# Optimization experiments

Hardware: AMD Instinct MI355X
Metric: run time of the kernel (lower is better)

The kernel has to match this reference:

```python
import jax, jax.numpy as jnp
import numpy as np
from functools import partial

N_NODES = 50000
N_EDGES = 600000
N_FEAT = 128
HID = [128, 64, 32, 16]
N_GRAPHS = 64
N_CLASSES = 10


def gcn_conv(x, W, b, src, dst, n_nodes):
    # PyG GCNConv: h = x @ W; propagate with symmetric norm over A + I; add bias.
    h = x @ W  # [N, out]
    ones = jnp.ones((src.shape[0],), dtype=x.dtype)
    deg = jax.ops.segment_sum(ones, dst, num_segments=n_nodes) + 1.0  # self-loop
    dinv = jax.lax.rsqrt(deg)
    coef = dinv[src] * dinv[dst]  # [E]
    agg = jax.ops.segment_sum(h[src] * coef[:, None], dst, num_segments=n_nodes)
    agg = agg + h * (dinv * dinv)[:, None]  # self-loop contribution
    return agg + b


def global_mean_pool(x, batch, n_graphs):
    s = jax.ops.segment_sum(x, batch, num_segments=n_graphs)
    cnt = jax.ops.segment_sum(jnp.ones((x.shape[0],), x.dtype), batch, num_segments=n_graphs)
    return s / jnp.maximum(cnt, 1.0)[:, None]


def setup_inputs() -> dict:
    key = jax.random.key(0)
    ks = jax.random.split(key, 16)
    x = jax.random.normal(ks[0], (N_NODES, N_FEAT), dtype=jnp.float32)
    edge_index = jax.random.randint(ks[1], (2, N_EDGES), 0, N_NODES, dtype=jnp.int64)
    batch = jnp.sort(jax.random.randint(ks[2], (N_NODES,), 0, N_GRAPHS, dtype=jnp.int64))

    def glorot(k, fan_in, fan_out):
        s = float(np.sqrt(6.0 / (fan_in + fan_out)))
        return jax.random.uniform(k, (fan_in, fan_out), jnp.float32, -s, s)

    dims = [N_FEAT] + HID
    params = {}
    for i in range(4):
        params[f"W{i+1}"] = glorot(ks[3 + i], dims[i], dims[i + 1])
        params[f"b{i+1}"] = jnp.zeros((dims[i + 1],), jnp.float32)
    params["Wlin"] = glorot(ks[7], HID[-1], N_CLASSES)
    params["blin"] = jnp.zeros((N_CLASSES,), jnp.float32)
    return {"x": x, "edge_index": edge_index, "batch": batch, **params}


def reference(x, edge_index, batch, W1, b1, W2, b2, W3, b3, W4, b4, Wlin, blin):
    src, dst = edge_index[0], edge_index[1]
    n = x.shape[0]
    h = jax.nn.relu(gcn_conv(x, W1, b1, src, dst, n))
    h = jax.nn.relu(gcn_conv(h, W2, b2, src, dst, n))
    h = jax.nn.relu(gcn_conv(h, W3, b3, src, dst, n))
    h = jax.nn.relu(gcn_conv(h, W4, b4, src, dst, n))
    g = global_mean_pool(h, batch, N_GRAPHS)  # [G, 16]
    return g @ Wlin + blin
```

## Files before the change

### kernel.cpp

```cpp
#include <hip/hip_runtime.h>
#include <hip/hip_bf16.h>


#define N_GRAPHS 64
#define N_CLASSES 10

typedef short bf8_t __attribute__((ext_vector_type(8)));
typedef float f4_t  __attribute__((ext_vector_type(4)));

__device__ __forceinline__ float b2f(unsigned int u) {
  return __uint_as_float(u << 16);
}
__device__ __forceinline__ unsigned short f2b(float f) {
  unsigned int x = __float_as_uint(f);
  x += 0x7fffu + ((x >> 16) & 1u);
  return (unsigned short)(x >> 16);
}

__device__ __forceinline__ void block_detect(const unsigned int* __restrict__ xraw,
    const unsigned int* __restrict__ eraw, int* f32, int* i64) {
  __shared__ int c_bf, c_nz;
  if (threadIdx.x == 0) { c_bf = 0; c_nz = 0; }
  __syncthreads();
  unsigned int d = xraw[threadIdx.x & 255];
  int e = (int)(((d & 0xffffu) >> 7) & 0xff);
  if (e >= 100 && e <= 140) atomicAdd(&c_bf, 1);
  if (eraw && threadIdx.x < 64 && eraw[2 * threadIdx.x + 1] != 0u) atomicAdd(&c_nz, 1);
  __syncthreads();
  *f32 = (c_bf < 150) ? 1 : 0;
  if (i64) *i64 = (c_nz == 0) ? 1 : 0;
}

struct WPtrs { const void* p[10]; };
static constexpr int WSEG[10] = {16384, 128, 8192, 64, 2048, 32, 512, 16, 160, 10};
static constexpr int WTOTAL   = 27546;
static constexpr int WOFF[10] = {0, 16384, 16512, 24704, 24768, 26816, 26848, 27360, 27376, 27536};

__global__ __launch_bounds__(256) void cvtwe_gemm1_kernel(
    const unsigned int* __restrict__ xraw, WPtrs wp, unsigned short* __restrict__ wc,
    const int* __restrict__ braw, int* __restrict__ b32,
    const int* __restrict__ eraw, int* __restrict__ deg, int* __restrict__ rank,
    unsigned short* __restrict__ H,
    int G1, int BW, int BB, int n, int E) {
  __shared__ unsigned short Wlds[16384];
  int f32, i64;
  block_detect(xraw, (const unsigned int*)eraw, &f32, &i64);
  const int bid = blockIdx.x;
  if (bid < G1) {
    const void* w1 = wp.p[0];
    #pragma unroll 4
    for (int it = 0; it < 64; ++it) {
      int srcI = it * 256 + threadIdx.x;
      int k = srcI >> 7, nn = srcI & 127;
      int kb = k >> 5, j = k & 7, quad = (k >> 3) & 3;
      int ct = nn >> 4, r16c = nn & 15;
      int l = quad * 16 + r16c;
      int f = ct * 4 + kb;
      unsigned short w = f32 ? f2b(((const float*)w1)[srcI])
                             : ((const unsigned short*)w1)[srcI];
      Wlds[(f * 64 + l) * 8 + j] = w;
    }
    __syncthreads();
    const int l = threadIdx.x & 63;
    const int r16 = l & 15, quad = l >> 4;
    const int m0 = (bid * 4 + (threadIdx.x >> 6)) * 32;
    if (m0 >= n) return;
    bf8_t afrag[2][4];
    #pragma unroll
    for (int mt = 0; mt < 2; ++mt) {
      int node = m0 + mt * 16 + r16;
      int nc = node < n ? node : n - 1;
      if (f32) {
        const float* xp = (const float*)xraw + (size_t)nc * 128 + quad * 8;
        #pragma unroll
        for (int kb = 0; kb < 4; ++kb) {
          const float4* p4 = (const float4*)(xp + kb * 32);
          float4 u0 = p4[0], u1 = p4[1];
          bf8_t a;
          a[0] = (short)f2b(u0.x); a[1] = (short)f2b(u0.y);
          a[2] = (short)f2b(u0.z); a[3] = (short)f2b(u0.w);
          a[4] = (short)f2b(u1.x); a[5] = (short)f2b(u1.y);
          a[6] = (short)f2b(u1.z); a[7] = (short)f2b(u1.w);
          afrag[mt][kb] = a;
        }
      } else {
        const unsigned short* xp = (const unsigned short*)xraw + (size_t)nc * 128 + quad * 8;
        #pragma unroll
        for (int kb = 0; kb < 4; ++kb)
          afrag[mt][kb] = *(const bf8_t*)(xp + kb * 32);
      }
    }
    #pragma unroll
    for (int ct = 0; ct < 8; ++ct) {
      bf8_t bfrag[4];
      #pragma unroll
      for (int kb = 0; kb < 4; ++kb)
        bfrag[kb] = *(const bf8_t*)(&Wlds[((ct * 4 + kb) * 64 + l) * 8]);
      #pragma unroll
      for (int mt = 0; mt < 2; ++mt) {
        f4_t acc = {0.f, 0.f, 0.f, 0.f};
        #pragma unroll
        for (int kb = 0; kb < 4; ++kb)
          acc = __builtin_amdgcn_mfma_f32_16x16x32_bf16(afrag[mt][kb], bfrag[kb], acc, 0, 0, 0);
        #pragma unroll
        for (int r = 0; r < 4; ++r) {
          int node = m0 + mt * 16 + quad * 4 + r;
          if (node < n)
            H[(size_t)node * 128 + ct * 16 + r16] = f2b(acc[r]);
        }
      }
    }
  } else if (bid < G1 + BW) {
    int i = (bid - G1) * 256 + threadIdx.x;
    if (i >= WTOTAL) return;
    int off = i, s = 0;
    #pragma unroll
    for (int t = 0; t < 10; ++t) {
      if (s == 0 && off >= WSEG[t]) { off -= WSEG[t]; } else if (s == 0) { s = t + 1; }
    }
    s -= 1;
    int soff = off;
    if ((s & 1) == 0 && s <= 6) {
      int KB, FOUT;
      if (s == 0)      { KB = 4; FOUT = 128; }
      else if (s == 2) { KB = 4; FOUT = 64; }
      else if (s == 4) { KB = 2; FOUT = 32; }
      else             { KB = 1; FOUT = 16; }
      int j = off & 7, l = (off >> 3) & 63, f = off >> 9;
      int ct = f / KB, kb = f - ct * KB;
      int k = kb * 32 + ((l >> 4) << 3) + j;
      int nn = ct * 16 + (l & 15);
      soff = k * FOUT + nn;
    }
    const void* p = wp.p[s];
    wc[WOFF[s] + off] = f32 ? f2b(((const float*)p)[soff])
                            : ((const unsigned short*)p)[soff];
  } else if (bid < G1 + BW + BB) {
    int i = (bid - G1 - BW) * 256 + threadIdx.x;
    if (i < n) b32[i] = i64 ? braw[2 * i] : braw[i];
  } else {
    int e = (bid - G1 - BW - BB) * 256 + threadIdx.x;
    if (e >= E) return;
    int d = i64 ? eraw[2 * (E + e)] : eraw[E + e];
    rank[e] = atomicAdd(&deg[(size_t)d << 4], 1);
  }
}

__global__ __launch_bounds__(256) void scan_kernel(const int* __restrict__ deg,
    int* __restrict__ row_ptr, float* __restrict__ dinv,
    unsigned long long* __restrict__ desc, int n) {
  __shared__ int ws[4];
  __shared__ int s_total;
  __shared__ unsigned int s_prev;
  const int b = blockIdx.x, tid = threadIdx.x, lane = tid & 63, wv = tid >> 6;
  const int i = b * 256 + tid;
  int v = (i < n) ? deg[(size_t)i << 4] : 0;
  int x = v;
  #pragma unroll
  for (int off = 1; off < 64; off <<= 1) {
    int y = __shfl_up(x, off, 64);
    if (lane >= off) x += y;
  }
  if (lane == 63) ws[wv] = x;
  __syncthreads();
  int wbase = 0;
  for (int w = 0; w < wv; ++w) wbase += ws[w];
  int incl = x + wbase;
  if (tid == 0) {
    int tot = ws[0] + ws[1] + ws[2] + ws[3];
    s_total = tot;
    unsigned long long st = (b == 0) ? (2ULL << 62) : (1ULL << 62);
    atomicExch(&desc[b], st | (unsigned long long)(unsigned int)tot);
    if (b == 0) s_prev = 0u;
  }
  __syncthreads();
  if (b > 0 && wv == 0) {
    unsigned int running = 0;
    int j = b - 1;
    while (true) {
      int idx = j - lane;
      unsigned long long d;
      if (idx >= 0) {
        do { d = atomicAdd(&desc[idx], 0ULL); } while ((d >> 62) == 0ULL);
      } else {
        d = (2ULL << 62);
      }
      unsigned long long ball = __ballot((d >> 62) == 2ULL);
      int fp = ball ? (__ffsll((unsigned long long)ball) - 1) : 64;
      unsigned int contrib = (lane <= fp) ? (unsigned int)(d & 0xffffffffULL) : 0u;
      #pragma unroll
      for (int o = 32; o; o >>= 1) contrib += __shfl_xor(contrib, o, 64);
      running += contrib;
      if (fp < 64) break;
      j -= 64;
    }
    if (lane == 0) {
      atomicExch(&desc[b], (2ULL << 62) |
                 (unsigned long long)(unsigned int)(running + (unsigned int)s_total));
      s_prev = running;
    }
  }
  __syncthreads();
  int tot = (int)s_prev + incl;
  if (i < n) {
    row_ptr[i + 1] = tot;
    dinv[i] = rsqrtf((float)v + 1.0f);
  }
  if (i == 0) row_ptr[0] = 0;
}

__global__ __launch_bounds__(256) void fill_kernel(
    const int* __restrict__ eraw, const unsigned int* __restrict__ xraw,
    const int* __restrict__ row_ptr, const int* __restrict__ rank,
    const float* __restrict__ dinv, uint2* __restrict__ csr, int E) {
  int f32, i64;
  block_detect(xraw, (const unsigned int*)eraw, &f32, &i64);
  int e = blockIdx.x * 256 + threadIdx.x;
  if (e >= E) return;
  int s, d;
  if (i64) { s = eraw[2 * e]; d = eraw[2 * (E + e)]; }
  else     { s = eraw[e];     d = eraw[E + e]; }
  int pos = row_ptr[d] + rank[e];
  uint2 v;
  v.x = (unsigned int)s;
  v.y = __float_as_uint(dinv[s] * dinv[d]);
  csr[pos] = v;
}

template<int DW> struct UVec { unsigned int d[DW]; };
template<int DW>
__device__ __forceinline__ UVec<DW> uload(const unsigned int* p) {
  UVec<DW> r;
  if constexpr (DW == 4) { uint4 v = *(const uint4*)p; r.d[0]=v.x; r.d[1]=v.y; r.d[2]=v.z; r.d[3]=v.w; }
  else if constexpr (DW == 2) { uint2 v = *(const uint2*)p; r.d[0]=v.x; r.d[1]=v.y; }
  else { r.d[0] = *p; }
  return r;
}
template<int DW>
__device__ __forceinline__ void ustore(unsigned int* p, const UVec<DW>& v) {
  if constexpr (DW == 4) { *(uint4*)p = make_uint4(v.d[0], v.d[1], v.d[2], v.d[3]); }
  else if constexpr (DW == 2) { *(uint2*)p = make_uint2(v.d[0], v.d[1]); }
  else { *p = v.d[0]; }
}

template<int FIN, int FOUT, int LPG>
__global__ __launch_bounds__(256) void aggemm_kernel(
    const unsigned short* __restrict__ Hin,
    const int* __restrict__ row_ptr, const uint2* __restrict__ csr,
    const float* __restrict__ dinv, const unsigned short* __restrict__ bias,
    const unsigned short* __restrict__ Wf, unsigned short* __restrict__ Hout, int n) {
  constexpr int DW  = FIN / LPG / 2;
  constexpr int NPB = 256 / LPG;
  constexpr int LD  = FIN + 8;
  constexpr int KB  = FIN / 32;
  constexpr int CT  = FOUT / 16;
  constexpr int MT  = NPB / 16;
  __shared__ unsigned short T[NPB * LD];
  const int r = threadIdx.x / LPG, l = threadIdx.x % LPG;
  const int node0 = blockIdx.x * NPB;
  const int g = node0 + r;
  const unsigned int* H2 = (const unsigned int*)Hin;
  UVec<DW> o;
  #pragma unroll
  for (int d = 0; d < DW; ++d) o.d[d] = 0u;
  if (g < n) {
    float di = dinv[g];
    float c0 = di * di;
    float a[2 * DW];
    UVec<DW> hv = uload<DW>(H2 + (size_t)g * (FIN / 2) + l * DW);
    #pragma unroll
    for (int d = 0; d < DW; ++d) {
      a[2*d]   = b2f(hv.d[d] & 0xffffu) * c0;
      a[2*d+1] = b2f(hv.d[d] >> 16) * c0;
    }
    const int e0 = row_ptr[g], e1 = row_ptr[g + 1];
    for (int base = e0; base < e1; base += LPG) {
      int cnt = e1 - base < LPG ? e1 - base : LPG;
      uint2 my = csr[(base + l < e1) ? (base + l) : (e1 - 1)];
      for (int j = 0; j < cnt; ++j) {
        int s = __shfl((int)my.x, j, LPG);
        float c = __uint_as_float(__shfl((int)my.y, j, LPG));
        UVec<DW> v = uload<DW>(H2 + (size_t)s * (FIN / 2) + l * DW);
        #pragma unroll
        for (int d = 0; d < DW; ++d) {
          a[2*d]   = fmaf(b2f(v.d[d] & 0xffffu), c, a[2*d]);
          a[2*d+1] = fmaf(b2f(v.d[d] >> 16), c, a[2*d+1]);
        }
      }
    }
    UVec<DW> bb = uload<DW>((const unsigned int*)bias + l * DW);
    #pragma unroll
    for (int d = 0; d < DW; ++d) {
      float lo = fmaxf(a[2*d]   + b2f(bb.d[d] & 0xffffu), 0.f);
      float hi = fmaxf(a[2*d+1] + b2f(bb.d[d] >> 16), 0.f);
      o.d[d] = (unsigned int)f2b(lo) | ((unsigned int)f2b(hi) << 16);
    }
  }
  ustore<DW>((unsigned int*)&T[r * LD + l * DW * 2], o);
  __syncthreads();
  const int w = threadIdx.x >> 6;
  if (w < MT * CT && node0 < n) {
    const int mt = w / CT, ct = w % CT;
    const int ll = threadIdx.x & 63;
    const int r16 = ll & 15, quad = ll >> 4;
    bf8_t afrag[KB], bfrag[KB];
    #pragma unroll
    for (int kb = 0; kb < KB; ++kb) {
      afrag[kb] = *(const bf8_t*)(&T[(mt * 16 + r16) * LD + quad * 8 + kb * 32]);
      bfrag[kb] = *(const bf8_t*)(Wf + ((ct * KB + kb) * 64 + ll) * 8);
    }
    f4_t acc = {0.f, 0.f, 0.f, 0.f};
    #pragma unroll
    for (int kb = 0; kb < KB; ++kb)
      acc = __builtin_amdgcn_mfma_f32_16x16x32_bf16(afrag[kb], bfrag[kb], acc, 0, 0, 0);
    #pragma unroll
    for (int rr = 0; rr < 4; ++rr) {
      int node = node0 + mt * 16 + quad * 4 + rr;
      if (node < n)
        Hout[(size_t)node * FOUT + ct * 16 + r16] = f2b(acc[rr]);
    }
  }
}

__global__ __launch_bounds__(256) void agg_pool_kernel(
    const unsigned short* __restrict__ Hin,
    const int* __restrict__ row_ptr, const uint2* __restrict__ csr,
    const float* __restrict__ dinv, const unsigned short* __restrict__ bias,
    const int* __restrict__ batch, float* __restrict__ pooled,
    float* __restrict__ cnt, int n) {
  __shared__ float acc[N_GRAPHS * 16];
  __shared__ float ccnt[N_GRAPHS];
  for (int i = threadIdx.x; i < N_GRAPHS * 16; i += 256) acc[i] = 0.f;
  if (threadIdx.x < N_GRAPHS) ccnt[threadIdx.x] = 0.f;
  __syncthreads();
  const int r = threadIdx.x >> 3, l = threadIdx.x & 7;
  const int g = blockIdx.x * 32 + r;
  if (g < n) {
    const unsigned int* H2 = (const unsigned int*)Hin;
    float di = dinv[g];
    float c0 = di * di;
    unsigned int hv = H2[(size_t)g * 8 + l];
    float a0 = b2f(hv & 0xffffu) * c0;
    float a1 = b2f(hv >> 16) * c0;
    const int e0 = row_ptr[g], e1 = row_ptr[g + 1];
    for (int base = e0; base < e1; base += 8) {
      int cnt2 = e1 - base < 8 ? e1 - base : 8;
      uint2 my = csr[(base + l < e1) ? (base + l) : (e1 - 1)];
      for (int j = 0; j < cnt2; ++j) {
        int s = __shfl((int)my.x, j, 8);
        float c = __uint_as_float(__shfl((int)my.y, j, 8));
        unsigned int v = H2[(size_t)s * 8 + l];
        a0 = fmaf(b2f(v & 0xffffu), c, a0);
        a1 = fmaf(b2f(v >> 16), c, a1);
      }
    }
    unsigned int bb = ((const unsigned int*)bias)[l];
    a0 = fmaxf(a0 + b2f(bb & 0xffffu), 0.f);
    a1 = fmaxf(a1 + b2f(bb >> 16), 0.f);
    int gb = batch[g];
    atomicAdd(&acc[gb * 16 + l * 2 + 0], a0);
    atomicAdd(&acc[gb * 16 + l * 2 + 1], a1);
    if (l == 0) atomicAdd(&ccnt[gb], 1.f);
  }
  __syncthreads();
  for (int i = threadIdx.x; i < N_GRAPHS * 16; i += 256)
    if (acc[i] != 0.f) atomicAdd(&pooled[i], acc[i]);
  if (threadIdx.x < N_GRAPHS && ccnt[threadIdx.x] != 0.f)
    atomicAdd(&cnt[threadIdx.x], ccnt[threadIdx.x]);
}

__global__ __launch_bounds__(256) void final_kernel(const float* __restrict__ pooled,
    const float* __restrict__ cnt, const unsigned short* __restrict__ wc,
    void* __restrict__ out, const unsigned int* __restrict__ xraw) {
  int f32;
  block_detect(xraw, nullptr, &f32, nullptr);
  int id = blockIdx.x * 256 + threadIdx.x;
  if (id >= N_GRAPHS * N_CLASSES) return;
  const unsigned short* Wlin = wc + WOFF[8];
  const unsigned short* blin = wc + WOFF[9];
  int g = id / N_CLASSES, c = id - g * N_CLASSES;
  float inv = 1.0f / fmaxf(cnt[g], 1.0f);
  float a = b2f(blin[c]);
  #pragma unroll
  for (int f = 0; f < 16; ++f)
    a = fmaf(pooled[g * 16 + f] * inv, b2f(Wlin[f * N_CLASSES + c]), a);
  if (f32) ((float*)out)[id] = a;
  else     ((unsigned short*)out)[id] = f2b(a);
}

extern "C" void kernel_launch(void* const* d_in, const int* in_sizes, int n_in,
                              void* d_out, int out_size, void* d_ws, size_t ws_size,
                              hipStream_t stream) {
  const unsigned int* xraw = (const unsigned int*)d_in[0];
  const int* eraw          = (const int*)d_in[1];
  const int* braw          = (const int*)d_in[2];

  const int N = in_sizes[2];
  const int E = in_sizes[1] / 2;
  const int nb = (N + 255) / 256;

  char* p = (char*)d_ws;
  auto alloc = [&](size_t bytes) -> void* {
    void* r = (void*)p;
    p += (bytes + 255) & ~(size_t)255;
    return r;
  };
  const size_t off_desc = ((size_t)N * 64 + 255) & ~(size_t)255;
  const size_t off_pool = (off_desc + (size_t)nb * 8 + 255) & ~(size_t)255;
  const size_t ztotal   = off_pool + (N_GRAPHS * 16 + N_GRAPHS) * 4;
  char* zbase = (char*)alloc(ztotal);
  int*   deg    = (int*)zbase;
  unsigned long long* desc = (unsigned long long*)(zbase + off_desc);
  float* pooled = (float*)(zbase + off_pool);
  float* cntf   = pooled + N_GRAPHS * 16;

  int*   row_ptr  = (int*)  alloc((size_t)(N + 1) * 4);
  int*   rank     = (int*)  alloc((size_t)E * 4);
  float* dinv     = (float*)alloc((size_t)N * 4);
  int*   batch32  = (int*)  alloc((size_t)N * 4);
  uint2* csr      = (uint2*)alloc((size_t)E * 8);
  unsigned short* wcan  = (unsigned short*)alloc((size_t)WTOTAL * 2);
  unsigned short* hbufA = (unsigned short*)alloc((size_t)N * 128 * 2);
  unsigned short* hbufB = (unsigned short*)alloc((size_t)N * 128 * 2);

  hipMemsetAsync(zbase, 0, ztotal, stream);

  WPtrs wp;
  for (int i = 0; i < 10; ++i) wp.p[i] = d_in[3 + i];

  const int BW = (WTOTAL + 255) / 256;
  const int BB = nb;
  const int BE = (E + 255) / 256;
  const int G1 = (N + 127) / 128;
  cvtwe_gemm1_kernel<<<G1 + BW + BB + BE, 256, 0, stream>>>(xraw, wp, wcan,
      braw, batch32, eraw, deg, rank, hbufA, G1, BW, BB, N, E);

  scan_kernel<<<nb, 256, 0, stream>>>(deg, row_ptr, dinv, desc, N);

  const unsigned short* b1 = wcan + WOFF[1];
  const unsigned short* W2 = wcan + WOFF[2];
  const unsigned short* b2 = wcan + WOFF[3];
  const unsigned short* W3 = wcan + WOFF[4];
  const unsigned short* b3 = wcan + WOFF[5];
  const unsigned short* W4 = wcan + WOFF[6];
  const unsigned short* b4 = wcan + WOFF[7];

  fill_kernel<<<BE, 256, 0, stream>>>(eraw, xraw, row_ptr, rank, dinv, csr, E);

  aggemm_kernel<128, 64, 16><<<(N + 15) / 16, 256, 0, stream>>>(
      hbufA, row_ptr, csr, dinv, b1, W2, hbufB, N);
  aggemm_kernel<64, 32, 8><<<(N + 31) / 32, 256, 0, stream>>>(
      hbufB, row_ptr, csr, dinv, b2, W3, hbufA, N);
  aggemm_kernel<32, 16, 8><<<(N + 31) / 32, 256, 0, stream>>>(
      hbufA, row_ptr, csr, dinv, b3, W4, hbufB, N);
  agg_pool_kernel<<<(N + 31) / 32, 256, 0, stream>>>(hbufB, row_ptr, csr, dinv, b4,
      batch32, pooled, cntf, N);

  final_kernel<<<(N_GRAPHS * N_CLASSES + 255) / 256, 256, 0, stream>>>(pooled, cntf, wcan, d_out, xraw);
}
```

Measured before the change: 226.8 us.

## Fold self-loops into CSR, MFMA layer-1 aggregation, slim W1 staging and degree counters

Self-loop entries are now written into the CSR by the scan kernel, so each node's row carries its own dinv^2 coefficient and the aggregation kernels no longer need a separate self-term or dinv read. The first aggregate+GEMM layer is replaced by an MFMA kernel that gathers 32 neighbour rows into LDS and builds a sparse coefficient A-matrix, so the weighted sum runs on matrix cores. The GEMM1 kernel now stages W1 one 16-column tile at a time in a small LDS buffer instead of the full matrix, trading extra syncs for lower LDS use and higher occupancy. The degree counters are no longer padded to 64 bytes and each edge block handles two edges per thread, which cuts the memset size but may add atomic contention.

New measurement: 227.3 us. Within noise of the previous version (+0.2%).

```diff
diff --git a/kernel.cpp b/kernel.cpp
--- a/kernel.cpp
+++ b/kernel.cpp
@@ -42,29 +42,15 @@
     const int* __restrict__ eraw, int* __restrict__ deg, int* __restrict__ rank,
     unsigned short* __restrict__ H,
     int G1, int BW, int BB, int n, int E) {
-  __shared__ unsigned short Wlds[16384];
+  __shared__ unsigned short Wlds2[2048];
   int f32, i64;
   block_detect(xraw, (const unsigned int*)eraw, &f32, &i64);
   const int bid = blockIdx.x;
   if (bid < G1) {
     const void* w1 = wp.p[0];
-    #pragma unroll 4
-    for (int it = 0; it < 64; ++it) {
-      int srcI = it * 256 + threadIdx.x;
-      int k = srcI >> 7, nn = srcI & 127;
-      int kb = k >> 5, j = k & 7, quad = (k >> 3) & 3;
-      int ct = nn >> 4, r16c = nn & 15;
-      int l = quad * 16 + r16c;
-      int f = ct * 4 + kb;
-      unsigned short w = f32 ? f2b(((const float*)w1)[srcI])
-                             : ((const unsigned short*)w1)[srcI];
-      Wlds[(f * 64 + l) * 8 + j] = w;
-    }
-    __syncthreads();
     const int l = threadIdx.x & 63;
     const int r16 = l & 15, quad = l >> 4;
     const int m0 = (bid * 4 + (threadIdx.x >> 6)) * 32;
-    if (m0 >= n) return;
     bf8_t afrag[2][4];
     #pragma unroll
     for (int mt = 0; mt < 2; ++mt) {
@@ -90,12 +76,31 @@
           afrag[mt][kb] = *(const bf8_t*)(xp + kb * 32);
       }
     }
-    #pragma unroll
     for (int ct = 0; ct < 8; ++ct) {
+      __syncthreads();
+      #pragma unroll
+      for (int it2 = 0; it2 < 2; ++it2) {
+        int seg = it2 * 64 + (threadIdx.x >> 2);
+        int c4  = threadIdx.x & 3;
+        int kb = seg >> 5, quadk = (seg >> 3) & 3, j = seg & 7;
+        int nnb = ct * 16 + c4 * 4;
+        unsigned short w4[4];
+        if (f32) {
+          float4 u = *(const float4*)((const float*)w1 + seg * 128 + nnb);
+          w4[0] = f2b(u.x); w4[1] = f2b(u.y); w4[2] = f2b(u.z); w4[3] = f2b(u.w);
+        } else {
+          ushort4 u = *(const ushort4*)((const unsigned short*)w1 + seg * 128 + nnb);
+          w4[0] = u.x; w4[1] = u.y; w4[2] = u.z; w4[3] = u.w;
+        }
+        #pragma unroll
+        for (int q4 = 0; q4 < 4; ++q4)
+          Wlds2[kb * 512 + (quadk * 16 + c4 * 4 + q4) * 8 + j] = w4[q4];
+      }
+      __syncthreads();
       bf8_t bfrag[4];
       #pragma unroll
       for (int kb = 0; kb < 4; ++kb)
-        bfrag[kb] = *(const bf8_t*)(&Wlds[((ct * 4 + kb) * 64 + l) * 8]);
+        bfrag[kb] = *(const bf8_t*)&Wlds2[kb * 512 + l * 8];
       #pragma unroll
       for (int mt = 0; mt < 2; ++mt) {
         f4_t acc = {0.f, 0.f, 0.f, 0.f};
@@ -139,22 +144,27 @@
     int i = (bid - G1 - BW) * 256 + threadIdx.x;
     if (i < n) b32[i] = i64 ? braw[2 * i] : braw[i];
   } else {
-    int e = (bid - G1 - BW - BB) * 256 + threadIdx.x;
-    if (e >= E) return;
-    int d = i64 ? eraw[2 * (E + e)] : eraw[E + e];
-    rank[e] = atomicAdd(&deg[(size_t)d << 4], 1);
+    int c = bid - G1 - BW - BB;
+    #pragma unroll
+    for (int r = 0; r < 2; ++r) {
+      int e = c * 512 + r * 256 + threadIdx.x;
+      if (e < E) {
+        int d = i64 ? eraw[2 * (E + e)] : eraw[E + e];
+        rank[e] = atomicAdd(&deg[d], 1);
+      }
+    }
   }
 }
 
 __global__ __launch_bounds__(256) void scan_kernel(const int* __restrict__ deg,
     int* __restrict__ row_ptr, float* __restrict__ dinv,
-    unsigned long long* __restrict__ desc, int n) {
+    unsigned long long* __restrict__ desc, uint2* __restrict__ csr, int n) {
   __shared__ int ws[4];
   __shared__ int s_total;
   __shared__ unsigned int s_prev;
   const int b = blockIdx.x, tid = threadIdx.x, lane = tid & 63, wv = tid >> 6;
   const int i = b * 256 + tid;
-  int v = (i < n) ? deg[(size_t)i << 4] : 0;
+  int v = (i < n) ? (deg[i] + 1) : 0;
   int x = v;
   #pragma unroll
   for (int off = 1; off < 64; off <<= 1) {
@@ -204,7 +214,12 @@
   int tot = (int)s_prev + incl;
   if (i < n) {
     row_ptr[i + 1] = tot;
-    dinv[i] = rsqrtf((float)v + 1.0f);
+    float di = rsqrtf((float)v);
+    dinv[i] = di;
+    uint2 se;
+    se.x = (unsigned int)i;
+    se.y = __float_as_uint(di * di);
+    csr[tot - v] = se;
   }
   if (i == 0) row_ptr[0] = 0;
 }
@@ -220,11 +235,99 @@
   int s, d;
   if (i64) { s = eraw[2 * e]; d = eraw[2 * (E + e)]; }
   else     { s = eraw[e];     d = eraw[E + e]; }
-  int pos = row_ptr[d] + rank[e];
+  int pos = row_ptr[d] + 1 + rank[e];
   uint2 v;
   v.x = (unsigned int)s;
   v.y = __float_as_uint(dinv[s] * dinv[d]);
   csr[pos] = v;
+}
+
+__global__ __launch_bounds__(256) void aggemm1_mfma_kernel(
+    const unsigned short* __restrict__ Hin,
+    const int* __restrict__ row_ptr, const uint2* __restrict__ csr,
+    const unsigned short* __restrict__ bias,
+    const unsigned short* __restrict__ Wf,
+    unsigned short* __restrict__ Hout, int n) {
+  __shared__ __align__(16) unsigned short Gf[8 * 544];
+  __shared__ __align__(16) unsigned short T[16 * 136];
+  __shared__ int rp[17];
+  __shared__ unsigned long long owner8[4];
+  __shared__ __align__(16) unsigned short coefh[32];
+  unsigned char* owner = (unsigned char*)owner8;
+  const int tid = threadIdx.x;
+  const int l = tid & 63, w = tid >> 6, l15 = l & 15, quad = l >> 4;
+  const int node0 = blockIdx.x * 16;
+  if (tid < 17) { int g = node0 + tid; rp[tid] = row_ptr[g < n ? g : n]; }
+  __syncthreads();
+  const int e0 = rp[0], e1 = rp[16];
+  f4_t acc0 = {0.f, 0.f, 0.f, 0.f}, acc1 = {0.f, 0.f, 0.f, 0.f};
+  const int s_slot = tid >> 3, qf = tid & 7;
+  for (int sb = e0; sb < e1; sb += 32) {
+    int gslot = sb + s_slot;
+    bool valid = gslot < e1;
+    uint2 ent = csr[valid ? gslot : e0];
+    if (qf == 0) {
+      float coef = valid ? __uint_as_float(ent.y) : 0.f;
+      int m = 0;
+      if (rp[m + 8] <= gslot) m += 8;
+      if (rp[m + 4] <= gslot) m += 4;
+      if (rp[m + 2] <= gslot) m += 2;
+      if (rp[m + 1] <= gslot) m += 1;
+      owner[s_slot] = (unsigned char)m;
+      coefh[s_slot] = f2b(coef);
+    }
+    const unsigned int* hp = (const unsigned int*)Hin + (size_t)ent.x * 64 + qf * 8;
+    uint4 v0 = *(const uint4*)hp;
+    uint4 v1 = *(const uint4*)(hp + 4);
+    unsigned int dws[8] = {v0.x, v0.y, v0.z, v0.w, v1.x, v1.y, v1.z, v1.w};
+    unsigned short* gb = &Gf[qf * 544 + (s_slot >> 3) * 136 + (s_slot & 7)];
+    #pragma unroll
+    for (int d2 = 0; d2 < 8; ++d2) {
+      gb[(d2 * 2) * 8]     = (unsigned short)(dws[d2] & 0xffffu);
+      gb[(d2 * 2 + 1) * 8] = (unsigned short)(dws[d2] >> 16);
+    }
+    __syncthreads();
+    unsigned long long ob = owner8[quad];
+    bf8_t cf = *(const bf8_t*)&coefh[quad * 8];
+    bf8_t af;
+    #pragma unroll
+    for (int j = 0; j < 8; ++j) {
+      int o = (int)((ob >> (8 * j)) & 0xffULL);
+      af[j] = (o == l15) ? cf[j] : (short)0;
+    }
+    {
+      const int ct = w * 2;
+      bf8_t bf0 = *(const bf8_t*)&Gf[ct * 544 + quad * 136 + l15 * 8];
+      acc0 = __builtin_amdgcn_mfma_f32_16x16x32_bf16(af, bf0, acc0, 0, 0, 0);
+      bf8_t bf1 = *(const bf8_t*)&Gf[(ct + 1) * 544 + quad * 136 + l15 * 8];
+      acc1 = __builtin_amdgcn_mfma_f32_16x16x32_bf16(af, bf1, acc1, 0, 0, 0);
+    }
+    __syncthreads();
+  }
+  {
+    const int ct = w * 2;
+    float bv0 = b2f(bias[ct * 16 + l15]);
+    float bv1 = b2f(bias[(ct + 1) * 16 + l15]);
+    #pragma unroll
+    for (int rr = 0; rr < 4; ++rr) {
+      T[(quad * 4 + rr) * 136 + ct * 16 + l15]       = f2b(fmaxf(acc0[rr] + bv0, 0.f));
+      T[(quad * 4 + rr) * 136 + (ct + 1) * 16 + l15] = f2b(fmaxf(acc1[rr] + bv1, 0.f));
+    }
+  }
+  __syncthreads();
+  f4_t a2 = {0.f, 0.f, 0.f, 0.f};
+  #pragma unroll
+  for (int kb = 0; kb < 4; ++kb) {
+    bf8_t afr = *(const bf8_t*)&T[l15 * 136 + kb * 32 + quad * 8];
+    bf8_t bfr = *(const bf8_t*)&Wf[((w * 4 + kb) * 64 + l) * 8];
+    a2 = __builtin_amdgcn_mfma_f32_16x16x32_bf16(afr, bfr, a2, 0, 0, 0);
+  }
+  #pragma unroll
+  for (int rr = 0; rr < 4; ++rr) {
+    int node = node0 + quad * 4 + rr;
+    if (node < n)
+      Hout[(size_t)node * 64 + w * 16 + l15] = f2b(a2[rr]);
+  }
 }
 
 template<int DW> struct UVec { unsigned int d[DW]; };
@@ -247,7 +350,7 @@
 __global__ __launch_bounds__(256) void aggemm_kernel(
     const unsigned short* __restrict__ Hin,
     const int* __restrict__ row_ptr, const uint2* __restrict__ csr,
-    const float* __restrict__ dinv, const unsigned short* __restrict__ bias,
+    const unsigned short* __restrict__ bias,
     const unsigned short* __restrict__ Wf, unsigned short* __restrict__ Hout, int n) {
   constexpr int DW  = FIN / LPG / 2;
   constexpr int NPB = 256 / LPG;
@@ -264,15 +367,9 @@
   #pragma unroll
   for (int d = 0; d < DW; ++d) o.d[d] = 0u;
   if (g < n) {
-    float di = dinv[g];
-    float c0 = di * di;
     float a[2 * DW];
-    UVec<DW> hv = uload<DW>(H2 + (size_t)g * (FIN / 2) + l * DW);
-    #pragma unroll
-    for (int d = 0; d < DW; ++d) {
-      a[2*d]   = b2f(hv.d[d] & 0xffffu) * c0;
-      a[2*d+1] = b2f(hv.d[d] >> 16) * c0;
-    }
+    #pragma unroll
+    for (int d = 0; d < 2 * DW; ++d) a[d] = 0.f;
     const int e0 = row_ptr[g], e1 = row_ptr[g + 1];
     for (int base = e0; base < e1; base += LPG) {
       int cnt = e1 - base < LPG ? e1 - base : LPG;
@@ -325,7 +422,7 @@
 __global__ __launch_bounds__(256) void agg_pool_kernel(
     const unsigned short* __restrict__ Hin,
     const int* __restrict__ row_ptr, const uint2* __restrict__ csr,
-    const float* __restrict__ dinv, const unsigned short* __restrict__ bias,
+    const unsigned short* __restrict__ bias,
     const int* __restrict__ batch, float* __restrict__ pooled,
     float* __restrict__ cnt, int n) {
   __shared__ float acc[N_GRAPHS * 16];
@@ -337,11 +434,7 @@
   const int g = blockIdx.x * 32 + r;
   if (g < n) {
     const unsigned int* H2 = (const unsigned int*)Hin;
-    float di = dinv[g];
-    float c0 = di * di;
-    unsigned int hv = H2[(size_t)g * 8 + l];
-    float a0 = b2f(hv & 0xffffu) * c0;
-    float a1 = b2f(hv >> 16) * c0;
+    float a0 = 0.f, a1 = 0.f;
     const int e0 = row_ptr[g], e1 = row_ptr[g + 1];
     for (int base = e0; base < e1; base += 8) {
       int cnt2 = e1 - base < 8 ? e1 - base : 8;
@@ -405,7 +498,7 @@
     p += (bytes + 255) & ~(size_t)255;
     return r;
   };
-  const size_t off_desc = ((size_t)N * 64 + 255) & ~(size_t)255;
+  const size_t off_desc = ((size_t)N * 4 + 255) & ~(size_t)255;
   const size_t off_pool = (off_desc + (size_t)nb * 8 + 255) & ~(size_t)255;
   const size_t ztotal   = off_pool + (N_GRAPHS * 16 + N_GRAPHS) * 4;
   char* zbase = (char*)alloc(ztotal);
@@ -418,7 +511,7 @@
   int*   rank     = (int*)  alloc((size_t)E * 4);
   float* dinv     = (float*)alloc((size_t)N * 4);
   int*   batch32  = (int*)  alloc((size_t)N * 4);
-  uint2* csr      = (uint2*)alloc((size_t)E * 8);
+  uint2* csr      = (uint2*)alloc((size_t)(E + N) * 8);
   unsigned short* wcan  = (unsigned short*)alloc((size_t)WTOTAL * 2);
   unsigned short* hbufA = (unsigned short*)alloc((size_t)N * 128 * 2);
   unsigned short* hbufB = (unsigned short*)alloc((size_t)N * 128 * 2);
@@ -428,14 +521,15 @@
   WPtrs wp;
   for (int i = 0; i < 10; ++i) wp.p[i] = d_in[3 + i];
 
-  const int BW = (WTOTAL + 255) / 256;
-  const int BB = nb;
-  const int BE = (E + 255) / 256;
-  const int G1 = (N + 127) / 128;
-  cvtwe_gemm1_kernel<<<G1 + BW + BB + BE, 256, 0, stream>>>(xraw, wp, wcan,
+  const int BW  = (WTOTAL + 255) / 256;
+  const int BB  = nb;
+  const int BE  = (E + 255) / 256;
+  const int BE2 = (E + 511) / 512;
+  const int G1  = (N + 127) / 128;
+  cvtwe_gemm1_kernel<<<G1 + BW + BB + BE2, 256, 0, stream>>>(xraw, wp, wcan,
       braw, batch32, eraw, deg, rank, hbufA, G1, BW, BB, N, E);
 
-  scan_kernel<<<nb, 256, 0, stream>>>(deg, row_ptr, dinv, desc, N);
+  scan_kernel<<<nb, 256, 0, stream>>>(deg, row_ptr, dinv, desc, csr, N);
 
   const unsigned short* b1 = wcan + WOFF[1];
   const unsigned short* W2 = wcan + WOFF[2];
@@ -447,13 +541,13 @@
 
   fill_kernel<<<BE, 256, 0, stream>>>(eraw, xraw, row_ptr, rank, dinv, csr, E);
 
-  aggemm_kernel<128, 64, 16><<<(N + 15) / 16, 256, 0, stream>>>(
-      hbufA, row_ptr, csr, dinv, b1, W2, hbufB, N);
+  aggemm1_mfma_kernel<<<(N + 15) / 16, 256, 0, stream>>>(
+      hbufA, row_ptr, csr, b1, W2, hbufB, N);
   aggemm_kernel<64, 32, 8><<<(N + 31) / 32, 256, 0, stream>>>(
-      hbufB, row_ptr, csr, dinv, b2, W3, hbufA, N);
+      hbufB, row_ptr, csr, b2, W3, hbufA, N);
   aggemm_kernel<32, 16, 8><<<(N + 31) / 32, 256, 0, stream>>>(
-      hbufA, row_ptr, csr, dinv, b3, W4, hbufB, N);
-  agg_pool_kernel<<<(N + 31) / 32, 256, 0, stream>>>(hbufB, row_ptr, csr, dinv, b4,
+      hbufA, row_ptr, csr, b3, W4, hbufB, N);
+  agg_pool_kernel<<<(N + 31) / 32, 256, 0, stream>>>(hbufB, row_ptr, csr, b4,
       batch32, pooled, cntf, N);
 
   final_kernel<<<(N_GRAPHS * N_CLASSES + 255) / 256, 256, 0, stream>>>(pooled, cntf, wcan, d_out, xraw);
```
